# Kernel tuning notes

Measured on AMD Instinct MI355X. Metric: run time of the kernel, lower is better.

Reference implementation:

```python
import jax, jax.numpy as jnp
import numpy as np


def setup_inputs() -> dict:
    key = jax.random.key(0)
    k1, k2 = jax.random.split(key)
    B, H, W, C = 128, 28, 28, 128
    x = jax.random.normal(k1, (B, H, W, C), dtype=jnp.float32)
    # template bank: [C, H, W, H, W] -- indexed by (channel, argmax_row, argmax_col)
    t_p = jax.random.uniform(k2, (C, H, W, H, W), dtype=jnp.float32)
    return {"x": x, "t_p": t_p}


def reference(x, t_p):
    B, H, W, C = x.shape
    # global spatial argmax per (batch, channel) == max_pool_with_argmax with ksize=(H,W)
    flat_idx = jnp.argmax(x.reshape(B, H * W, C), axis=1)  # [B, C]
    h = flat_idx // W  # [B, C]
    w = flat_idx % W   # [B, C]
    c_idx = jnp.arange(C)[None, :]  # [1, C] broadcast against [B, C]
    # gather per-(b,c) template: t_p[c, h*, w*, :, :] -> [B, C, H, W]
    templates = t_p[c_idx, h, w]  # [B, C, H, W]
    templates = jnp.transpose(templates, (0, 2, 3, 1))  # [B, H, W, C]
    masked = jax.nn.relu(x * templates)
    return (masked, x, templates)
```

## Files before the change

kernel.cpp:

```cpp
#include <hip/hip_runtime.h>


constexpr int HWc = 784, Cc = 128, Bc = 128;

typedef float f4 __attribute__((ext_vector_type(4)));
typedef int i4 __attribute__((ext_vector_type(4)));

__device__ inline void nt_store(float* p, f4 v) {
  __builtin_nontemporal_store(v, (f4*)p);
}

__global__ __launch_bounds__(256) void argmax_part_kernel(
    const float* __restrict__ x, float* __restrict__ pmax,
    int* __restrict__ pidx) {
  int blk = blockIdx.x;
  int b = blk >> 1;
  int chunk = blk & 1;
  int t = threadIdx.x;
  int c4 = t & 31;
  int part = t >> 5;
  int s0 = chunk * 392 + part * 49;

  const float* xp = x + (size_t)b * HWc * Cc + (c4 << 2);
  const f4* p = (const f4*)(xp + (size_t)s0 * Cc);

  f4 best = {-3.4e38f, -3.4e38f, -3.4e38f, -3.4e38f};
  i4 bi = {s0, s0, s0, s0};
  for (int k = 0; k < 49; ++k) {
    f4 v = *p;
    p += Cc / 4;
    int s = s0 + k;
    if (v[0] > best[0]) { best[0] = v[0]; bi[0] = s; }
    if (v[1] > best[1]) { best[1] = v[1]; bi[1] = s; }
    if (v[2] > best[2]) { best[2] = v[2]; bi[2] = s; }
    if (v[3] > best[3]) { best[3] = v[3]; bi[3] = s; }
  }

  __shared__ float smax[8][Cc];
  __shared__ int sidx[8][Cc];
  *(f4*)&smax[part][c4 << 2] = best;
  *(i4*)&sidx[part][c4 << 2] = bi;
  __syncthreads();

  if (t < Cc) {
    float m = smax[0][t];
    int mi = sidx[0][t];
#pragma unroll
    for (int pp = 1; pp < 8; ++pp) {
      float v = smax[pp][t];
      if (v > m) { m = v; mi = sidx[pp][t]; }
    }
    int o = (b * 2 + chunk) * Cc + t;
    pmax[o] = m;
    pidx[o] = mi;
  }
}

__global__ __launch_bounds__(256) void fused_out_kernel(
    const float* __restrict__ x, const float* __restrict__ tp,
    const float* __restrict__ pmax, const int* __restrict__ pidx,
    float* __restrict__ out) {
  int b = blockIdx.y;
  int t = threadIdx.x;

  __shared__ int tbase[Cc];
  if (t < Cc) {
    int base = b * 2 * Cc + t;
    float m = pmax[base];
    int mi = pidx[base];
    float v = pmax[base + Cc];
    if (v > m) { m = v; mi = pidx[base + Cc]; }
    tbase[t] = (t * HWc + mi) * HWc;
  }
  __syncthreads();

  int c4 = t & 31;
  int u = t >> 5;
  int ch = c4 << 2;

  const float* r0 = tp + tbase[ch + 0];
  const float* r1 = tp + tbase[ch + 1];
  const float* r2 = tp + tbase[ch + 2];
  const float* r3 = tp + tbase[ch + 3];

  const size_t plane = (size_t)HWc * Cc;
  size_t bplane = (size_t)b * plane;
  float* om = out;
  float* ox = out + (size_t)Bc * plane;
  float* ot = out + 2 * (size_t)Bc * plane;
  int sb = blockIdx.x * 112;

  for (int k = 0; k < 4; ++k) {
    int idx = 8 * k + u;
    if (idx < 28) {
      int s0 = sb + (idx << 2);
      size_t off = bplane + (size_t)s0 * Cc + ch;
      const float* xp = x + off;

      f4 xv0 = *(const f4*)(xp);
      f4 xv1 = *(const f4*)(xp + Cc);
      f4 xv2 = *(const f4*)(xp + 2 * Cc);
      f4 xv3 = *(const f4*)(xp + 3 * Cc);
      f4 tv0 = *(const f4*)(r0 + s0);
      f4 tv1 = *(const f4*)(r1 + s0);
      f4 tv2 = *(const f4*)(r2 + s0);
      f4 tv3 = *(const f4*)(r3 + s0);

      float* omp = om + off;
      float* oxp = ox + off;
      float* otp = ot + off;

#pragma unroll
      for (int i = 0; i < 4; ++i) {
        f4 xvi = (i == 0) ? xv0 : (i == 1) ? xv1 : (i == 2) ? xv2 : xv3;
        f4 tcol = {tv0[i], tv1[i], tv2[i], tv3[i]};
        f4 mv;
        mv[0] = fmaxf(xvi[0] * tcol[0], 0.f);
        mv[1] = fmaxf(xvi[1] * tcol[1], 0.f);
        mv[2] = fmaxf(xvi[2] * tcol[2], 0.f);
        mv[3] = fmaxf(xvi[3] * tcol[3], 0.f);
        nt_store(omp + i * Cc, mv);
        nt_store(oxp + i * Cc, xvi);
        nt_store(otp + i * Cc, tcol);
      }
    }
  }
}

extern "C" void kernel_launch(void* const* d_in, const int* in_sizes, int n_in,
                              void* d_out, int out_size, void* d_ws,
                              size_t ws_size, hipStream_t stream) {
  const float* x = (const float*)d_in[0];
  const float* tp = (const float*)d_in[1];
  float* out = (float*)d_out;

  float* pmax = (float*)d_ws;
  int* pidx = (int*)((char*)d_ws + (size_t)Bc * 2 * Cc * sizeof(float));

  argmax_part_kernel<<<dim3(Bc * 2), 256, 0, stream>>>(x, pmax, pidx);
  fused_out_kernel<<<dim3(7, Bc), 256, 0, stream>>>(x, tp, pmax, pidx, out);
}
```

Before: 57.76 us.

## Fuse argmax and output kernels into one 1024-thread kernel per batch half

Merges the partial-argmax kernel and the output kernel into one kernel. Each 1024-thread block computes the full per-batch argmax over all 784 positions, then writes its half of the spatial outputs. This removes a launch and the workspace round trip. In exchange, each batch's argmax is computed twice (once per half-block), x is read one extra time, and only 256 large blocks are launched. Template loads also become nontemporal.

```diff
diff --git a/kernel.cpp b/kernel.cpp
--- a/kernel.cpp
+++ b/kernel.cpp
@@ -9,91 +9,72 @@
 __device__ inline void nt_store(float* p, f4 v) {
   __builtin_nontemporal_store(v, (f4*)p);
 }
+__device__ inline f4 nt_load(const float* p) {
+  return __builtin_nontemporal_load((const f4*)p);
+}
 
-__global__ __launch_bounds__(256) void argmax_part_kernel(
-    const float* __restrict__ x, float* __restrict__ pmax,
-    int* __restrict__ pidx) {
-  int blk = blockIdx.x;
-  int b = blk >> 1;
-  int chunk = blk & 1;
+__global__ __launch_bounds__(1024) void fused_kernel(
+    const float* __restrict__ x, const float* __restrict__ tp,
+    float* __restrict__ out) {
+  int half = blockIdx.x;
+  int b = blockIdx.y;
   int t = threadIdx.x;
   int c4 = t & 31;
-  int part = t >> 5;
-  int s0 = chunk * 392 + part * 49;
+  int g = t >> 5;
+  int ch = c4 << 2;
 
-  const float* xp = x + (size_t)b * HWc * Cc + (c4 << 2);
-  const f4* p = (const f4*)(xp + (size_t)s0 * Cc);
+  const size_t plane = (size_t)HWc * Cc;
+  size_t bplane = (size_t)b * plane;
 
-  f4 best = {-3.4e38f, -3.4e38f, -3.4e38f, -3.4e38f};
-  i4 bi = {s0, s0, s0, s0};
-  for (int k = 0; k < 49; ++k) {
-    f4 v = *p;
-    p += Cc / 4;
-    int s = s0 + k;
-    if (v[0] > best[0]) { best[0] = v[0]; bi[0] = s; }
-    if (v[1] > best[1]) { best[1] = v[1]; bi[1] = s; }
-    if (v[2] > best[2]) { best[2] = v[2]; bi[2] = s; }
-    if (v[3] > best[3]) { best[3] = v[3]; bi[3] = s; }
+  __shared__ float smax[32][Cc];
+  __shared__ int sidx[32][Cc];
+  __shared__ int tbase[Cc];
+
+  {
+    int s0 = g * 25;
+    int send = (s0 + 25 < HWc) ? (s0 + 25) : HWc;
+    const f4* p = (const f4*)(x + bplane + (size_t)s0 * Cc + ch);
+    f4 best = {-3.4e38f, -3.4e38f, -3.4e38f, -3.4e38f};
+    i4 bi = {s0, s0, s0, s0};
+    for (int s = s0; s < send; ++s) {
+      f4 v = *p;
+      p += Cc / 4;
+      if (v[0] > best[0]) { best[0] = v[0]; bi[0] = s; }
+      if (v[1] > best[1]) { best[1] = v[1]; bi[1] = s; }
+      if (v[2] > best[2]) { best[2] = v[2]; bi[2] = s; }
+      if (v[3] > best[3]) { best[3] = v[3]; bi[3] = s; }
+    }
+    *(f4*)&smax[g][ch] = best;
+    *(i4*)&sidx[g][ch] = bi;
   }
-
-  __shared__ float smax[8][Cc];
-  __shared__ int sidx[8][Cc];
-  *(f4*)&smax[part][c4 << 2] = best;
-  *(i4*)&sidx[part][c4 << 2] = bi;
   __syncthreads();
 
   if (t < Cc) {
     float m = smax[0][t];
     int mi = sidx[0][t];
 #pragma unroll
-    for (int pp = 1; pp < 8; ++pp) {
-      float v = smax[pp][t];
-      if (v > m) { m = v; mi = sidx[pp][t]; }
+    for (int p = 1; p < 32; ++p) {
+      float v = smax[p][t];
+      if (v > m) { m = v; mi = sidx[p][t]; }
     }
-    int o = (b * 2 + chunk) * Cc + t;
-    pmax[o] = m;
-    pidx[o] = mi;
-  }
-}
-
-__global__ __launch_bounds__(256) void fused_out_kernel(
-    const float* __restrict__ x, const float* __restrict__ tp,
-    const float* __restrict__ pmax, const int* __restrict__ pidx,
-    float* __restrict__ out) {
-  int b = blockIdx.y;
-  int t = threadIdx.x;
-
-  __shared__ int tbase[Cc];
-  if (t < Cc) {
-    int base = b * 2 * Cc + t;
-    float m = pmax[base];
-    int mi = pidx[base];
-    float v = pmax[base + Cc];
-    if (v > m) { m = v; mi = pidx[base + Cc]; }
     tbase[t] = (t * HWc + mi) * HWc;
   }
   __syncthreads();
-
-  int c4 = t & 31;
-  int u = t >> 5;
-  int ch = c4 << 2;
 
   const float* r0 = tp + tbase[ch + 0];
   const float* r1 = tp + tbase[ch + 1];
   const float* r2 = tp + tbase[ch + 2];
   const float* r3 = tp + tbase[ch + 3];
 
-  const size_t plane = (size_t)HWc * Cc;
-  size_t bplane = (size_t)b * plane;
   float* om = out;
   float* ox = out + (size_t)Bc * plane;
   float* ot = out + 2 * (size_t)Bc * plane;
-  int sb = blockIdx.x * 112;
+  int sbase = half * 392;
 
   for (int k = 0; k < 4; ++k) {
-    int idx = 8 * k + u;
-    if (idx < 28) {
-      int s0 = sb + (idx << 2);
+    int idx = g + (k << 5);
+    if (idx < 98) {
+      int s0 = sbase + (idx << 2);
       size_t off = bplane + (size_t)s0 * Cc + ch;
       const float* xp = x + off;
 
@@ -101,10 +82,10 @@
       f4 xv1 = *(const f4*)(xp + Cc);
       f4 xv2 = *(const f4*)(xp + 2 * Cc);
       f4 xv3 = *(const f4*)(xp + 3 * Cc);
-      f4 tv0 = *(const f4*)(r0 + s0);
-      f4 tv1 = *(const f4*)(r1 + s0);
-      f4 tv2 = *(const f4*)(r2 + s0);
-      f4 tv3 = *(const f4*)(r3 + s0);
+      f4 tv0 = nt_load(r0 + s0);
+      f4 tv1 = nt_load(r1 + s0);
+      f4 tv2 = nt_load(r2 + s0);
+      f4 tv3 = nt_load(r3 + s0);
 
       float* omp = om + off;
       float* oxp = ox + off;
@@ -133,10 +114,5 @@
   const float* x = (const float*)d_in[0];
   const float* tp = (const float*)d_in[1];
   float* out = (float*)d_out;
-
-  float* pmax = (float*)d_ws;
-  int* pidx = (int*)((char*)d_ws + (size_t)Bc * 2 * Cc * sizeof(float));
-
-  argmax_part_kernel<<<dim3(Bc * 2), 256, 0, stream>>>(x, pmax, pidx);
-  fused_out_kernel<<<dim3(7, Bc), 256, 0, stream>>>(x, tp, pmax, pidx, out);
+  fused_kernel<<<dim3(2, Bc), 1024, 0, stream>>>(x, tp, out);
 }
```

Measured after the change: 81.48 us. 41.1% more time.

## Move x passthrough copy into argmax kernel and rebalance both grids

Applied to the files above, without the earlier changes.

The copy of x to the second output now happens in the first (argmax) kernel, which already reads all of x, so the second kernel writes only the masked and template outputs. The argmax kernel uses 512 threads with 16 partitions of 25 rows each. The output kernel doubles its grid (14 column blocks of 56 positions each) to spread less work per block. The aim is to balance store traffic across the two kernels, with more parallelism in the first kernel, which previously only read.

```diff
diff --git a/kernel.cpp b/kernel.cpp
--- a/kernel.cpp
+++ b/kernel.cpp
@@ -10,45 +10,49 @@
   __builtin_nontemporal_store(v, (f4*)p);
 }
 
-__global__ __launch_bounds__(256) void argmax_part_kernel(
-    const float* __restrict__ x, float* __restrict__ pmax,
-    int* __restrict__ pidx) {
-  int blk = blockIdx.x;
-  int b = blk >> 1;
-  int chunk = blk & 1;
+__global__ __launch_bounds__(512) void argmax_copy_kernel(
+    const float* __restrict__ x, float* __restrict__ ox,
+    float* __restrict__ pmax, int* __restrict__ pidx) {
+  int chunk = blockIdx.x;
+  int b = blockIdx.y;
   int t = threadIdx.x;
   int c4 = t & 31;
   int part = t >> 5;
-  int s0 = chunk * 392 + part * 49;
+  int ch = c4 << 2;
 
-  const float* xp = x + (size_t)b * HWc * Cc + (c4 << 2);
-  const f4* p = (const f4*)(xp + (size_t)s0 * Cc);
+  int cbase = chunk * 392;
+  int s0 = cbase + part * 25;
+  int send = s0 + 25;
+  if (send > cbase + 392) send = cbase + 392;
+
+  const size_t plane = (size_t)HWc * Cc;
+  const float* xp = x + (size_t)b * plane + ch;
+  float* oxp = ox + (size_t)b * plane + ch;
 
   f4 best = {-3.4e38f, -3.4e38f, -3.4e38f, -3.4e38f};
   i4 bi = {s0, s0, s0, s0};
-  for (int k = 0; k < 49; ++k) {
-    f4 v = *p;
-    p += Cc / 4;
-    int s = s0 + k;
+  for (int s = s0; s < send; ++s) {
+    f4 v = *(const f4*)(xp + (size_t)s * Cc);
+    nt_store(oxp + (size_t)s * Cc, v);
     if (v[0] > best[0]) { best[0] = v[0]; bi[0] = s; }
     if (v[1] > best[1]) { best[1] = v[1]; bi[1] = s; }
     if (v[2] > best[2]) { best[2] = v[2]; bi[2] = s; }
     if (v[3] > best[3]) { best[3] = v[3]; bi[3] = s; }
   }
 
-  __shared__ float smax[8][Cc];
-  __shared__ int sidx[8][Cc];
-  *(f4*)&smax[part][c4 << 2] = best;
-  *(i4*)&sidx[part][c4 << 2] = bi;
+  __shared__ float smax[16][Cc];
+  __shared__ int sidx[16][Cc];
+  *(f4*)&smax[part][ch] = best;
+  *(i4*)&sidx[part][ch] = bi;
   __syncthreads();
 
   if (t < Cc) {
     float m = smax[0][t];
     int mi = sidx[0][t];
 #pragma unroll
-    for (int pp = 1; pp < 8; ++pp) {
-      float v = smax[pp][t];
-      if (v > m) { m = v; mi = sidx[pp][t]; }
+    for (int p = 1; p < 16; ++p) {
+      float v = smax[p][t];
+      if (v > m) { m = v; mi = sidx[p][t]; }
     }
     int o = (b * 2 + chunk) * Cc + t;
     pmax[o] = m;
@@ -56,7 +60,7 @@
   }
 }
 
-__global__ __launch_bounds__(256) void fused_out_kernel(
+__global__ __launch_bounds__(256) void out_kernel(
     const float* __restrict__ x, const float* __restrict__ tp,
     const float* __restrict__ pmax, const int* __restrict__ pidx,
     float* __restrict__ out) {
@@ -86,13 +90,13 @@
   const size_t plane = (size_t)HWc * Cc;
   size_t bplane = (size_t)b * plane;
   float* om = out;
-  float* ox = out + (size_t)Bc * plane;
   float* ot = out + 2 * (size_t)Bc * plane;
-  int sb = blockIdx.x * 112;
+  int sb = blockIdx.x * 56;
 
-  for (int k = 0; k < 4; ++k) {
-    int idx = 8 * k + u;
-    if (idx < 28) {
+#pragma unroll
+  for (int k = 0; k < 2; ++k) {
+    int idx = u + (k << 3);
+    if (idx < 14) {
       int s0 = sb + (idx << 2);
       size_t off = bplane + (size_t)s0 * Cc + ch;
       const float* xp = x + off;
@@ -107,7 +111,6 @@
       f4 tv3 = *(const f4*)(r3 + s0);
 
       float* omp = om + off;
-      float* oxp = ox + off;
       float* otp = ot + off;
 
 #pragma unroll
@@ -120,7 +123,6 @@
         mv[2] = fmaxf(xvi[2] * tcol[2], 0.f);
         mv[3] = fmaxf(xvi[3] * tcol[3], 0.f);
         nt_store(omp + i * Cc, mv);
-        nt_store(oxp + i * Cc, xvi);
         nt_store(otp + i * Cc, tcol);
       }
     }
@@ -133,10 +135,11 @@
   const float* x = (const float*)d_in[0];
   const float* tp = (const float*)d_in[1];
   float* out = (float*)d_out;
+  float* ox = out + (size_t)Bc * HWc * Cc;
 
   float* pmax = (float*)d_ws;
   int* pidx = (int*)((char*)d_ws + (size_t)Bc * 2 * Cc * sizeof(float));
 
-  argmax_part_kernel<<<dim3(Bc * 2), 256, 0, stream>>>(x, pmax, pidx);
-  fused_out_kernel<<<dim3(7, Bc), 256, 0, stream>>>(x, tp, pmax, pidx, out);
+  argmax_copy_kernel<<<dim3(2, Bc), 512, 0, stream>>>(x, ox, pmax, pidx);
+  out_kernel<<<dim3(14, Bc), 256, 0, stream>>>(x, tp, pmax, pidx, out);
 }
```

New measurement: 56.95 us. About the same (-1.4%).
